# Optimization experiments

Measured on AMD Instinct MI355X. Metric: run time of the kernel, lower is better.

The kernel has to match this reference:

```python
import jax, jax.numpy as jnp
import numpy as np

B, C, H, W = 2, 256, 120, 240
HID = 512  # mlp_ratio=2 * embed_dim
EPS = 1e-5


def setup_inputs() -> dict:
    key = jax.random.key(0)
    ks = jax.random.split(key, 10)
    f = lambda k, shp, s=1.0: jax.random.normal(k, shp, jnp.float32) * s
    return {
        'x': f(ks[0], (B, C, H, W)),
        'gamma': f(ks[1], (C,), 0.1),
        'beta': f(ks[2], (C,), 0.1),
        'norm0_w': jnp.ones((C,), jnp.float32),
        'norm0_b': jnp.zeros((C,), jnp.float32),
        'norm1_w': jnp.ones((C,), jnp.float32),
        'norm1_b': jnp.zeros((C,), jnp.float32),
        'w_spec_r': f(ks[3], (C, C), 0.02),
        'w_spec_i': f(ks[4], (C, C), 0.02),
        'inner_w': f(ks[5], (C, C), 0.02),
        'inner_b': jnp.zeros((C,), jnp.float32),
        'mlp_w1': f(ks[6], (HID, C), 0.02),
        'mlp_b1': jnp.zeros((HID,), jnp.float32),
        'mlp_w2': f(ks[7], (C, HID), 0.02),
        'mlp_b2': jnp.zeros((C,), jnp.float32),
    }


def _inorm(x, w, b):
    # InstanceNorm2d (affine): normalize over spatial dims per (batch, channel)
    m = x.mean(axis=(2, 3), keepdims=True)
    v = x.var(axis=(2, 3), keepdims=True)
    xh = (x - m) * jax.lax.rsqrt(v + EPS)
    return xh * w[None, :, None, None] + b[None, :, None, None]


def _conv1x1(x, w, b=None):
    y = jnp.einsum('bihw,oi->bohw', x, w)
    return y if b is None else y + b[None, :, None, None]


def reference(x, gamma, beta, norm0_w, norm0_b, norm1_w, norm1_b,
              w_spec_r, w_spec_i, inner_w, inner_b,
              mlp_w1, mlp_b1, mlp_w2, mlp_b2):
    residual = x
    h = _inorm(x, norm0_w, norm0_b)
    # SpectralConv2d: rfft2 -> channel-mixing complex matmul (all modes kept,
    # hard_thresholding_fraction=1.0) -> irfft2. sparsity_threshold=0 -> no shrink.
    xf = jnp.fft.rfft2(h, norm='ortho')                     # [B,C,H,W//2+1] complex
    wc = (w_spec_r + 1j * w_spec_i).astype(xf.dtype)
    yf = jnp.einsum('bihw,io->bohw', xf, wc)
    h = jnp.fft.irfft2(yf, s=(H, W), norm='ortho')
    # inner skip (1x1 conv of residual) + GELU (linear filter branch)
    h = h + _conv1x1(residual, inner_w, inner_b)
    h = jax.nn.gelu(h, approximate=False)
    h = _inorm(h, norm1_w, norm1_b)
    # FiLM with scale=1
    h = (1.0 + gamma[None, :, None, None]) * h + beta[None, :, None, None]
    # distributed MLP: 1x1 conv -> GELU -> 1x1 conv
    h = _conv1x1(h, mlp_w1, mlp_b1)
    h = jax.nn.gelu(h, approximate=False)
    h = _conv1x1(h, mlp_w2, mlp_b2)
    # outer skip = identity
    return h + residual
```

## Files before the change

### kernel.cpp

```cpp
#include <hip/hip_runtime.h>
#include <hip/hip_bf16.h>

typedef __hip_bfloat16 bf16;
typedef short short8 __attribute__((ext_vector_type(8)));
typedef float f32x4 __attribute__((ext_vector_type(4)));

#define NB 2
#define NC 256
#define NH 120
#define NW 240
#define NHW (NH*NW)
#define NSP 16384
#define NHID 512
#define NPT 450
#define REPS 1e-5f
#define SC_W 0.06454972243679028f
#define SC_H 0.09128709291752769f
#define PI2 6.283185307179586f

__device__ __forceinline__ float gelu_f(float x){ return 0.5f*x*(1.f+erff(x*0.7071067811865476f)); }
__device__ __forceinline__ float us2f(ushort u){ union{float f; uint v;} c; c.v=((uint)u)<<16; return c.f; }
__device__ __forceinline__ ushort f2us(float f){ bf16 b=__float2bfloat16(f); return *(ushort*)&b; }

#define OFF_A0   0
#define OFF_D0   512
#define OFF_A1c  1024
#define OFF_D1c  1536
#define OFF_TWF  2048
#define OFF_THF  34816
#define OFF_THI  67584
#define OFF_TWI  100352
#define OFF_WRT  133120
#define OFF_WIT  165888
#define OFF_IWB  198656
#define OFF_W2B  231424
#define OFF_W1P  296960
#define OFF_B1P  428032
#define OFF_PS   429056
#define OFF_RA   889856
#define OFF_RB   9278464
#define WS_FLOATS 17667072ULL

#define RA0 OFF_RA
#define RA1 (OFF_RA+4194304)
#define RB0 OFF_RB
#define RB1 (OFF_RB+4194304)
#define OFF_FRE RB0
#define OFF_FIM (RB0+3932160)

__global__ __launch_bounds__(256) void k_setup(float* ws, const float* wsr, const float* wsi,
                                               const float* iw, const float* w2){
  int t = blockIdx.x*256 + threadIdx.x;
  if (t < 65536){
    int n=t>>8, w=t&255; float v=0.f;
    if(w<NW){
      if(n<121){ v = cosf(PI2*(float)((n*w)%NW)/(float)NW)*SC_W; }
      else if(n>=128 && n<249){ int k=n-128; v = -sinf(PI2*(float)((k*w)%NW)/(float)NW)*SC_W; }
    }
    ((ushort*)(ws+OFF_TWF))[t]=f2us(v); return;
  } t-=65536;
  if (t < 65536){
    int n=t>>8, j=t&255; float v=0.f;
    int h = j&127; bool im = (j>=128);
    if(h<NH){
      if(n<128){ int m=n; if(m<NH){ float sn,cs; sincosf(PI2*(float)((m*h)%NH)/(float)NH,&sn,&cs);
        v = (im? sn : cs)*SC_H; } }
      else { int m=n-128; if(m<NH){ float sn,cs; sincosf(PI2*(float)((m*h)%NH)/(float)NH,&sn,&cs);
        v = (im? cs : -sn)*SC_H; } }
    }
    ((ushort*)(ws+OFF_THF))[t]=f2us(v); return;
  } t-=65536;
  if (t < 65536){
    int n=t>>8, j=t&255; float v=0.f;
    int m = j&127; bool im = (j>=128);
    if(m<NH){
      if(n<128){ int h=n; if(h<NH){ float sn,cs; sincosf(PI2*(float)((h*m)%NH)/(float)NH,&sn,&cs);
        v = (im? -sn : cs)*SC_H; } }
      else { int h=n-128; if(h<NH){ float sn,cs; sincosf(PI2*(float)((h*m)%NH)/(float)NH,&sn,&cs);
        v = (im? cs : sn)*SC_H; } }
    }
    ((ushort*)(ws+OFF_THI))[t]=f2us(v); return;
  } t-=65536;
  if (t < 65536){
    int w=t>>8, j=t&255; float v=0.f;
    if(w<NW){
      int k = j&127; bool im = (j>=128);
      if(k<121){
        float ck = (k==0||k==120)? 1.f : 2.f;
        float sn,cs; sincosf(PI2*(float)((w*k)%NW)/(float)NW,&sn,&cs);
        v = ck*(im? -sn : cs)*SC_W;
      }
    }
    ((ushort*)(ws+OFF_TWI))[t]=f2us(v); return;
  } t-=65536;
  if (t < 65536){ int o=t>>8,i=t&255; ((ushort*)(ws+OFF_WRT))[t]=f2us(wsr[i*NC+o]); return; } t-=65536;
  if (t < 65536){ int o=t>>8,i=t&255; ((ushort*)(ws+OFF_WIT))[t]=f2us(wsi[i*NC+o]); return; } t-=65536;
  if (t < 65536){ ((ushort*)(ws+OFF_IWB))[t]=f2us(iw[t]); return; } t-=65536;
  if (t < 131072){ ((ushort*)(ws+OFF_W2B))[t]=f2us(w2[t]); return; }
}

__global__ __launch_bounds__(256) void k_stats0(const float* x, const float* n0w, const float* n0b, float* ws){
  int g = blockIdx.x, c = g & (NC-1);
  const float4* xp = (const float4*)(x + (size_t)g*NHW);
  float s=0.f, q=0.f;
  for(int i=threadIdx.x;i<NHW/4;i+=256){
    float4 v=xp[i];
    s+=v.x+v.y+v.z+v.w;
    q=fmaf(v.x,v.x,fmaf(v.y,v.y,fmaf(v.z,v.z,fmaf(v.w,v.w,q))));
  }
  __shared__ float ls[4], lq[4];
  #pragma unroll
  for(int o=32;o>0;o>>=1){ s+=__shfl_down(s,o,64); q+=__shfl_down(q,o,64); }
  int lane=threadIdx.x&63, wid=threadIdx.x>>6;
  if(!lane){ ls[wid]=s; lq[wid]=q; }
  __syncthreads();
  if(!threadIdx.x){
    s=ls[0]+ls[1]+ls[2]+ls[3]; q=lq[0]+lq[1]+lq[2]+lq[3];
    float m=s*(1.f/NHW), var=q*(1.f/NHW)-m*m;
    float r=rsqrtf(var+REPS);
    float a=r*n0w[c];
    ws[OFF_A0+g]=a; ws[OFF_D0+g]=fmaf(-m,a,n0b[c]);
  }
}

__global__ __launch_bounds__(256) void k_norm(const float* x, float* ws){
  int h = blockIdx.x, g = blockIdx.y, t = threadIdx.x;
  float a = ws[OFF_A0+g], d = ws[OFF_D0+g];
  ushort v = 0;
  if(t < NW) v = f2us(fmaf(a, x[(size_t)g*NHW + (size_t)h*NW + t], d));
  ((ushort*)(ws+RA0))[(size_t)g*30720 + (size_t)h*256 + t] = v;
}

template<int SPLIT, int EPI>
__global__ __launch_bounds__(256) void k_sgemm(const ushort* Ap0, const ushort* Ap1, const ushort* Bm,
                                               ushort* O0, ushort* O1, ushort* Ub){
  int nb = blockIdx.x*64, mb = blockIdx.y*256;
  int tid = threadIdx.x, w = tid>>6, l = tid&63, lq = l>>4, lr = l&15;
  const ushort* ar0[4]; const ushort* ar1[4]; const ushort* br[4];
  #pragma unroll
  for(int mt=0;mt<4;mt++){
    size_t r = mb + w*64 + mt*16 + lr;
    ar0[mt] = Ap0 + r*(SPLIT?128:256) + lq*8;
    ar1[mt] = SPLIT ? (Ap1 + r*128 + lq*8) : ar0[mt];
  }
  #pragma unroll
  for(int nt=0;nt<4;nt++) br[nt] = Bm + (size_t)(nb + nt*16 + lr)*256 + lq*8;
  f32x4 acc[4][4] = {};
  #pragma unroll
  for(int kk=0;kk<8;kk++){
    int k = kk*32;
    short8 af[4], bfr[4];
    #pragma unroll
    for(int mt=0;mt<4;mt++){
      const ushort* p = SPLIT ? ((k<128 ? ar0[mt] : ar1[mt]) + (k&127)) : (ar0[mt] + k);
      af[mt] = *(const short8*)p;
    }
    #pragma unroll
    for(int nt=0;nt<4;nt++) bfr[nt] = *(const short8*)(br[nt]+k);
    #pragma unroll
    for(int mt=0;mt<4;mt++)
      #pragma unroll
      for(int nt=0;nt<4;nt++)
        acc[mt][nt] = __builtin_amdgcn_mfma_f32_16x16x32_bf16(af[mt], bfr[nt], acc[mt][nt], 0,0,0);
  }
  #pragma unroll
  for(int mt=0;mt<4;mt++){
    #pragma unroll
    for(int r=0;r<4;r++){
      int m = mb + w*64 + mt*16 + lq*4 + r;
      #pragma unroll
      for(int nt=0;nt<4;nt++){
        int n = nb + nt*16 + lr;
        float v = acc[mt][nt][r];
        if (EPI==0){
          if(n<128) O0[(size_t)m*128+n] = f2us(v);
          else      O1[(size_t)m*128+n-128] = f2us(v);
        } else {
          int g = m>>7, h = m&127;
          if(h<NH && n<NW) Ub[(size_t)g*NHW + (size_t)h*NW + n] = f2us(v);
        }
      }
    }
  }
}

__global__ __launch_bounds__(256) void k_t64(const ushort* src, ushort* dst, int srows, int sgstr){
  __shared__ ushort lt[64][72];
  int g=blockIdx.z, i0=blockIdx.y*64, p0=blockIdx.x*64;
  int t=threadIdx.x, r=t>>2, q=t&3;
  int row = i0 + r;
  uint4 u0=make_uint4(0,0,0,0), u1=u0;
  if(row < srows){
    const ushort* sp = src + (size_t)g*sgstr + (size_t)row*128 + p0 + q*16;
    u0=*(const uint4*)sp; u1=*(const uint4*)(sp+8);
  }
  *(uint4*)&lt[r][q*16]=u0; *(uint4*)&lt[r][q*16+8]=u1;
  __syncthreads();
  int pr=t>>2, q2=t&3;
  union { ushort s[8]; uint4 u; } o0, o1;
  #pragma unroll
  for(int e=0;e<8;e++){ o0.s[e]=lt[q2*16+e][pr]; o1.s[e]=lt[q2*16+8+e][pr]; }
  ushort* dp = dst + (size_t)g*NSP + (size_t)(p0+pr)*128 + i0 + q2*16;
  *(uint4*)dp = o0.u; *(uint4*)(dp+8) = o1.u;
}

__global__ __launch_bounds__(256) void k_tP(const ushort* src, ushort* dst){
  __shared__ ushort lt[64][72];
  int b=blockIdx.z, i0=blockIdx.y*64, p0=blockIdx.x*64;
  int t=threadIdx.x, r=t>>2, q=t&3;
  const ushort* sp = src + (size_t)(b*NC+i0+r)*NSP + p0 + q*16;
  uint4 u0=*(const uint4*)sp, u1=*(const uint4*)(sp+8);
  *(uint4*)&lt[r][q*16]=u0; *(uint4*)&lt[r][q*16+8]=u1;
  __syncthreads();
  int pr=t>>2, q2=t&3;
  union { ushort s[8]; uint4 u; } o0, o1;
  #pragma unroll
  for(int e=0;e<8;e++){ o0.s[e]=lt[q2*16+e][pr]; o1.s[e]=lt[q2*16+8+e][pr]; }
  ushort* dp = dst + ((size_t)b*NSP + p0 + pr)*NC + i0 + q2*16;
  *(uint4*)dp = o0.u; *(uint4*)(dp+8) = o1.u;
}

__global__ __launch_bounds__(256) void k_mixg(float* ws){
  int b = blockIdx.z, p0 = blockIdx.x*32;
  int tid = threadIdx.x, w = tid>>6, l = tid&63, lq = l>>4, lr = l&15;
  const ushort* Wr = (const ushort*)(ws+OFF_WRT);
  const ushort* Wi = (const ushort*)(ws+OFF_WIT);
  const ushort* Gr = (const ushort*)(ws+RA0) + (size_t)b*NSP*NC;
  const ushort* Gi = (const ushort*)(ws+RA1) + (size_t)b*NSP*NC;
  const ushort *wrr[4], *wir[4], *brr[2], *bir[2];
  #pragma unroll
  for(int mt=0;mt<4;mt++){ size_t ro=(size_t)(w*64+mt*16+lr)*NC+lq*8; wrr[mt]=Wr+ro; wir[mt]=Wi+ro; }
  #pragma unroll
  for(int nt=0;nt<2;nt++){ size_t ro=(size_t)(p0+nt*16+lr)*NC+lq*8; brr[nt]=Gr+ro; bir[nt]=Gi+ro; }
  f32x4 aR[4][2]={}, aI[4][2]={};
  for(int k=0;k<256;k+=32){
    short8 fr[4], fi[4], fin[4], gr[2], gi[2];
    #pragma unroll
    for(int mt=0;mt<4;mt++){
      fr[mt]=*(const short8*)(wrr[mt]+k);
      fi[mt]=*(const short8*)(wir[mt]+k);
      union { short8 s; uint u[4]; } nv; nv.s=fi[mt];
      nv.u[0]^=0x80008000u; nv.u[1]^=0x80008000u; nv.u[2]^=0x80008000u; nv.u[3]^=0x80008000u;
      fin[mt]=nv.s;
    }
    #pragma unroll
    for(int nt=0;nt<2;nt++){ gr[nt]=*(const short8*)(brr[nt]+k); gi[nt]=*(const short8*)(bir[nt]+k); }
    #pragma unroll
    for(int mt=0;mt<4;mt++)
      #pragma unroll
      for(int nt=0;nt<2;nt++){
        aR[mt][nt]=__builtin_amdgcn_mfma_f32_16x16x32_bf16(fr[mt], gr[nt], aR[mt][nt],0,0,0);
        aR[mt][nt]=__builtin_amdgcn_mfma_f32_16x16x32_bf16(fin[mt],gi[nt], aR[mt][nt],0,0,0);
        aI[mt][nt]=__builtin_amdgcn_mfma_f32_16x16x32_bf16(fi[mt], gr[nt], aI[mt][nt],0,0,0);
        aI[mt][nt]=__builtin_amdgcn_mfma_f32_16x16x32_bf16(fr[mt], gi[nt], aI[mt][nt],0,0,0);
      }
  }
  ushort* Yre = (ushort*)(ws+RB0);
  ushort* Yim = (ushort*)(ws+RB1);
  #pragma unroll
  for(int mt=0;mt<4;mt++){
    #pragma unroll
    for(int r=0;r<4;r++){
      int m = w*64 + mt*16 + lq*4 + r;
      #pragma unroll
      for(int nt=0;nt<2;nt++){
        int n = p0 + nt*16 + lr;
        size_t ad = (size_t)(b*NC+m)*NSP + n;
        Yre[ad] = f2us(aR[mt][nt][r]);
        Yim[ad] = f2us(aI[mt][nt][r]);
      }
    }
  }
}

__global__ __launch_bounds__(256,2) void k_inner(float* ws, const float* x, const float* ib){
  __shared__ ushort xt[64][264];
  int b = blockIdx.z, blk = blockIdx.x, p0 = blk*64;
  int t = threadIdx.x, w = t>>6, l = t&63, lq = l>>4, lr = l&15;
  #pragma unroll 4
  for(int cc=0; cc<16; cc++){
    int c = cc*16 + (t>>4);
    int p4 = (t&15)*4;
    float4 v = *(const float4*)(x + ((size_t)(b*NC+c))*NHW + p0 + p4);
    xt[p4  ][c]=f2us(v.x); xt[p4+1][c]=f2us(v.y);
    xt[p4+2][c]=f2us(v.z); xt[p4+3][c]=f2us(v.w);
  }
  __syncthreads();
  const ushort* W = (const ushort*)(ws+OFF_IWB);
  const ushort* ar[4];
  #pragma unroll
  for(int mt=0;mt<4;mt++) ar[mt] = W + (size_t)(w*64+mt*16+lr)*256 + lq*8;
  f32x4 acc[4][4] = {};
  #pragma unroll
  for(int kk=0;kk<8;kk++){
    int k = kk*32;
    short8 af[4], bfr[4];
    #pragma unroll
    for(int mt=0;mt<4;mt++) af[mt] = *(const short8*)(ar[mt]+k);
    #pragma unroll
    for(int nt=0;nt<4;nt++) bfr[nt] = *(const short8*)&xt[nt*16+lr][k+lq*8];
    #pragma unroll
    for(int mt=0;mt<4;mt++)
      #pragma unroll
      for(int nt=0;nt<4;nt++)
        acc[mt][nt] = __builtin_amdgcn_mfma_f32_16x16x32_bf16(af[mt], bfr[nt], acc[mt][nt], 0,0,0);
  }
  __syncthreads();
  const ushort* Usp = (const ushort*)(ws+OFF_RA);
  float* PS = ws + OFF_PS + ((size_t)(b*NPT+blk))*512;
  #pragma unroll
  for(int mt=0;mt<4;mt++){
    #pragma unroll
    for(int r=0;r<4;r++){
      int m = w*64 + mt*16 + lq*4 + r;
      float bb = ib[m];
      float ss = 0.f, sq = 0.f;
      #pragma unroll
      for(int nt=0;nt<4;nt++){
        int n = p0 + nt*16 + lr;
        float uv = us2f(Usp[((size_t)(b*NC+m))*NHW + n]);
        float g = gelu_f(acc[mt][nt][r] + bb + uv);
        xt[nt*16+lr][m] = f2us(g);
        ss += g; sq = fmaf(g,g,sq);
      }
      #pragma unroll
      for(int ofs=1; ofs<16; ofs<<=1){ ss += __shfl_xor(ss, ofs, 64); sq += __shfl_xor(sq, ofs, 64); }
      if(lr==0){ PS[m] = ss; PS[256+m] = sq; }
    }
  }
  __syncthreads();
  ushort* Up = (ushort*)(ws+OFF_RB);
  #pragma unroll
  for(int pp=0; pp<4; pp++){
    int p = pp*16 + (t>>4);
    int c0 = (t&15)*16;
    uint4 w0 = *(uint4*)&xt[p][c0];
    uint4 w1v = *(uint4*)&xt[p][c0+8];
    ushort* dp = Up + ((size_t)(b*NHW + p0 + p))*256 + c0;
    *(uint4*)dp = w0; *(uint4*)(dp+8) = w1v;
  }
}

__global__ __launch_bounds__(256) void k_stats1p(const float* gamma, const float* beta,
                                                 const float* n1w, const float* n1b, float* ws){
  int g = blockIdx.x, b = g>>8, c = g&255;
  float s=0.f, q=0.f;
  for(int i=threadIdx.x;i<NPT;i+=256){
    const float* P = ws + OFF_PS + ((size_t)(b*NPT+i))*512;
    s += P[c]; q += P[256+c];
  }
  __shared__ float ls[4], lq2[4];
  #pragma unroll
  for(int o=32;o>0;o>>=1){ s+=__shfl_down(s,o,64); q+=__shfl_down(q,o,64); }
  int lane=threadIdx.x&63, wid=threadIdx.x>>6;
  if(!lane){ ls[wid]=s; lq2[wid]=q; }
  __syncthreads();
  if(!threadIdx.x){
    s=ls[0]+ls[1]+ls[2]+ls[3]; q=lq2[0]+lq2[1]+lq2[2]+lq2[3];
    float m=s*(1.f/NHW), var=q*(1.f/NHW)-m*m;
    float r=rsqrtf(var+REPS);
    float gp1 = 1.f + gamma[c];
    float wv = n1w[c];
    ws[OFF_A1c+g] = gp1*wv*r;
    ws[OFF_D1c+g] = gp1*(n1b[c] - m*r*wv) + beta[c];
  }
}

__global__ __launch_bounds__(64) void k_fold(float* ws, const float* w1, const float* b1){
  int o = blockIdx.x, b = blockIdx.y, t = threadIdx.x;
  float acc = 0.f;
  ushort* W1p = (ushort*)(ws+OFF_W1P);
  #pragma unroll
  for(int ii=0; ii<4; ii++){
    int i = ii*64 + t;
    float wv = w1[o*256+i];
    W1p[((size_t)(b*NHID+o))*256 + i] = f2us(wv * ws[OFF_A1c + b*NC + i]);
    acc = fmaf(wv, ws[OFF_D1c + b*NC + i], acc);
  }
  #pragma unroll
  for(int ofs=32; ofs; ofs>>=1) acc += __shfl_down(acc, ofs, 64);
  if(!t) ws[OFF_B1P + b*NHID + o] = acc + b1[o];
}

__global__ __launch_bounds__(256,2) void k_mlp(float* ws, const float* x, const float* b2, float* out){
  __shared__ ushort midT[64][520];
  int b = blockIdx.z, p0 = blockIdx.x*64;
  int t = threadIdx.x, w = t>>6, l = t&63, lq = l>>4, lr = l&15;
  const ushort* W1p = (const ushort*)(ws+OFF_W1P) + (size_t)b*NHID*256;
  const ushort* Up  = (const ushort*)(ws+OFF_RB);
  const ushort* ar[8]; const ushort* br[4];
  #pragma unroll
  for(int mt=0;mt<8;mt++) ar[mt] = W1p + (size_t)(w*128+mt*16+lr)*256 + lq*8;
  #pragma unroll
  for(int nt=0;nt<4;nt++) br[nt] = Up + ((size_t)(b*NHW + p0 + nt*16+lr))*256 + lq*8;
  f32x4 acc1[8][4] = {};
  #pragma unroll
  for(int kk=0;kk<8;kk++){
    int k = kk*32;
    short8 bfr[4];
    #pragma unroll
    for(int nt=0;nt<4;nt++) bfr[nt] = *(const short8*)(br[nt]+k);
    #pragma unroll
    for(int mt=0;mt<8;mt++){
      short8 af = *(const short8*)(ar[mt]+k);
      #pragma unroll
      for(int nt=0;nt<4;nt++)
        acc1[mt][nt] = __builtin_amdgcn_mfma_f32_16x16x32_bf16(af, bfr[nt], acc1[mt][nt], 0,0,0);
    }
  }
  const float* b1p = ws + OFF_B1P + b*NHID;
  #pragma unroll
  for(int mt=0;mt<8;mt++){
    #pragma unroll
    for(int r=0;r<4;r++){
      int m1 = w*128 + mt*16 + lq*4 + r;
      float bb = b1p[m1];
      #pragma unroll
      for(int nt=0;nt<4;nt++){
        int p = nt*16 + lr;
        midT[p][m1] = f2us(gelu_f(acc1[mt][nt][r] + bb));
      }
    }
  }
  __syncthreads();
  const ushort* W2 = (const ushort*)(ws+OFF_W2B);
  const ushort* a2[4];
  #pragma unroll
  for(int mt=0;mt<4;mt++) a2[mt] = W2 + (size_t)(w*64+mt*16+lr)*512 + lq*8;
  f32x4 acc2[4][4] = {};
  #pragma unroll
  for(int kk=0;kk<16;kk++){
    int k = kk*32;
    short8 af[4], bfr[4];
    #pragma unroll
    for(int mt=0;mt<4;mt++) af[mt] = *(const short8*)(a2[mt]+k);
    #pragma unroll
    for(int nt=0;nt<4;nt++) bfr[nt] = *(const short8*)&midT[nt*16+lr][k+lq*8];
    #pragma unroll
    for(int mt=0;mt<4;mt++)
      #pragma unroll
      for(int nt=0;nt<4;nt++)
        acc2[mt][nt] = __builtin_amdgcn_mfma_f32_16x16x32_bf16(af[mt], bfr[nt], acc2[mt][nt], 0,0,0);
  }
  #pragma unroll
  for(int mt=0;mt<4;mt++){
    #pragma unroll
    for(int r=0;r<4;r++){
      int om = w*64 + mt*16 + lq*4 + r;
      float bb = b2[om];
      #pragma unroll
      for(int nt=0;nt<4;nt++){
        int n = p0 + nt*16 + lr;
        size_t ad = ((size_t)(b*NC+om))*NHW + n;
        out[ad] = acc2[mt][nt][r] + bb + x[ad];
      }
    }
  }
}

extern "C" void kernel_launch(void* const* d_in, const int* in_sizes, int n_in,
                              void* d_out, int out_size, void* d_ws, size_t ws_size,
                              hipStream_t stream) {
  const float* x     = (const float*)d_in[0];
  const float* gamma = (const float*)d_in[1];
  const float* beta  = (const float*)d_in[2];
  const float* n0w   = (const float*)d_in[3];
  const float* n0b   = (const float*)d_in[4];
  const float* n1w   = (const float*)d_in[5];
  const float* n1b   = (const float*)d_in[6];
  const float* wsr   = (const float*)d_in[7];
  const float* wsi   = (const float*)d_in[8];
  const float* iw    = (const float*)d_in[9];
  const float* ib    = (const float*)d_in[10];
  const float* w1    = (const float*)d_in[11];
  const float* b1    = (const float*)d_in[12];
  const float* w2    = (const float*)d_in[13];
  const float* b2    = (const float*)d_in[14];
  float* ws = (float*)d_ws;
  float* out = (float*)d_out;
  if (ws_size < WS_FLOATS*4ULL) return;

  k_setup <<<dim3(2304), dim3(256), 0, stream>>>(ws, wsr, wsi, iw, w2);
  k_stats0<<<dim3(512),  dim3(256), 0, stream>>>(x, n0w, n0b, ws);
  k_norm  <<<dim3(120,512), dim3(256), 0, stream>>>(x, ws);
  k_sgemm<0,0><<<dim3(4,240), dim3(256), 0, stream>>>((const ushort*)(ws+RA0), (const ushort*)(ws+RA0),
      (const ushort*)(ws+OFF_TWF), (ushort*)(ws+OFF_FRE), (ushort*)(ws+OFF_FIM), nullptr);
  k_t64 <<<dim3(2,2,512), dim3(256), 0, stream>>>((const ushort*)(ws+OFF_FRE), (ushort*)(ws+RA0), NH, NH*128);
  k_t64 <<<dim3(2,2,512), dim3(256), 0, stream>>>((const ushort*)(ws+OFF_FIM), (ushort*)(ws+RA1), NH, NH*128);
  k_sgemm<1,0><<<dim3(4,256), dim3(256), 0, stream>>>((const ushort*)(ws+RA0), (const ushort*)(ws+RA1),
      (const ushort*)(ws+OFF_THF), (ushort*)(ws+RB0), (ushort*)(ws+RB1), nullptr);
  k_tP <<<dim3(256,4,2), dim3(256), 0, stream>>>((const ushort*)(ws+RB0), (ushort*)(ws+RA0));
  k_tP <<<dim3(256,4,2), dim3(256), 0, stream>>>((const ushort*)(ws+RB1), (ushort*)(ws+RA1));
  k_mixg <<<dim3(512,1,2), dim3(256), 0, stream>>>(ws);
  k_sgemm<1,0><<<dim3(4,256), dim3(256), 0, stream>>>((const ushort*)(ws+RB0), (const ushort*)(ws+RB1),
      (const ushort*)(ws+OFF_THI), (ushort*)(ws+RA0), (ushort*)(ws+RA1), nullptr);
  k_t64 <<<dim3(2,2,512), dim3(256), 0, stream>>>((const ushort*)(ws+RA0), (ushort*)(ws+RB0), 128, NSP);
  k_t64 <<<dim3(2,2,512), dim3(256), 0, stream>>>((const ushort*)(ws+RA1), (ushort*)(ws+RB1), 128, NSP);
  k_sgemm<1,1><<<dim3(4,256), dim3(256), 0, stream>>>((const ushort*)(ws+RB0), (const ushort*)(ws+RB1),
      (const ushort*)(ws+OFF_TWI), nullptr, nullptr, (ushort*)(ws+RA0));
  k_inner <<<dim3(NPT,1,2), dim3(256), 0, stream>>>(ws, x, ib);
  k_stats1p<<<dim3(512), dim3(256), 0, stream>>>(gamma, beta, n1w, n1b, ws);
  k_fold  <<<dim3(512,2), dim3(64), 0, stream>>>(ws, w1, b1);
  k_mlp   <<<dim3(NPT,1,2), dim3(256), 0, stream>>>(ws, x, b2, out);
}
```

Before: 648.8 us.

## Fuse MLP stages in registers, dropping the shared-memory intermediate

```diff
diff --git a/kernel.cpp b/kernel.cpp
--- a/kernel.cpp
+++ b/kernel.cpp
@@ -96,7 +96,12 @@
   if (t < 65536){ int o=t>>8,i=t&255; ((ushort*)(ws+OFF_WRT))[t]=f2us(wsr[i*NC+o]); return; } t-=65536;
   if (t < 65536){ int o=t>>8,i=t&255; ((ushort*)(ws+OFF_WIT))[t]=f2us(wsi[i*NC+o]); return; } t-=65536;
   if (t < 65536){ ((ushort*)(ws+OFF_IWB))[t]=f2us(iw[t]); return; } t-=65536;
-  if (t < 131072){ ((ushort*)(ws+OFF_W2B))[t]=f2us(w2[t]); return; }
+  if (t < 131072){
+    int o = t>>9, k = t&511;
+    int kp = (k & ~31) | ((k&4)<<2) | ((k>>1)&12) | (k&3);
+    ((ushort*)(ws+OFF_W2B))[t]=f2us(w2[(o<<9)+kp]);
+    return;
+  }
 }
 
 __global__ __launch_bounds__(256) void k_stats0(const float* x, const float* n0w, const float* n0b, float* ws){
@@ -382,78 +387,49 @@
   if(!t) ws[OFF_B1P + b*NHID + o] = acc + b1[o];
 }
 
-__global__ __launch_bounds__(256,2) void k_mlp(float* ws, const float* x, const float* b2, float* out){
-  __shared__ ushort midT[64][520];
+__global__ __launch_bounds__(256,4) void k_mlp(float* ws, const float* x, const float* b2, float* out){
   int b = blockIdx.z, p0 = blockIdx.x*64;
   int t = threadIdx.x, w = t>>6, l = t&63, lq = l>>4, lr = l&15;
+  int pw = p0 + w*16 + lr;
   const ushort* W1p = (const ushort*)(ws+OFF_W1P) + (size_t)b*NHID*256;
   const ushort* Up  = (const ushort*)(ws+OFF_RB);
-  const ushort* ar[8]; const ushort* br[4];
-  #pragma unroll
-  for(int mt=0;mt<8;mt++) ar[mt] = W1p + (size_t)(w*128+mt*16+lr)*256 + lq*8;
-  #pragma unroll
-  for(int nt=0;nt<4;nt++) br[nt] = Up + ((size_t)(b*NHW + p0 + nt*16+lr))*256 + lq*8;
-  f32x4 acc1[8][4] = {};
-  #pragma unroll
-  for(int kk=0;kk<8;kk++){
-    int k = kk*32;
-    short8 bfr[4];
-    #pragma unroll
-    for(int nt=0;nt<4;nt++) bfr[nt] = *(const short8*)(br[nt]+k);
-    #pragma unroll
-    for(int mt=0;mt<8;mt++){
-      short8 af = *(const short8*)(ar[mt]+k);
-      #pragma unroll
-      for(int nt=0;nt<4;nt++)
-        acc1[mt][nt] = __builtin_amdgcn_mfma_f32_16x16x32_bf16(af, bfr[nt], acc1[mt][nt], 0,0,0);
-    }
-  }
-  const float* b1p = ws + OFF_B1P + b*NHID;
-  #pragma unroll
-  for(int mt=0;mt<8;mt++){
+  const float*  b1p = ws + OFF_B1P + b*NHID;
+  const ushort* up  = Up + ((size_t)(b*NHW) + pw)*256 + lq*8;
+  const ushort* w2r = (const ushort*)(ws+OFF_W2B) + (size_t)lr*512 + lq*8;
+  f32x4 acc2[16] = {};
+  for(int c=0;c<16;c++){
+    const ushort* w1r = W1p + (size_t)(c*32 + lr)*256 + lq*8;
+    f32x4 a1[2] = {};
+    #pragma unroll
+    for(int kk=0;kk<8;kk++){
+      short8 bu  = *(const short8*)(up  + kk*32);
+      short8 a0  = *(const short8*)(w1r + kk*32);
+      short8 a1f = *(const short8*)(w1r + 16*256 + kk*32);
+      a1[0] = __builtin_amdgcn_mfma_f32_16x16x32_bf16(a0,  bu, a1[0], 0,0,0);
+      a1[1] = __builtin_amdgcn_mfma_f32_16x16x32_bf16(a1f, bu, a1[1], 0,0,0);
+    }
+    float4 bb0 = *(const float4*)(b1p + c*32      + lq*4);
+    float4 bb1 = *(const float4*)(b1p + c*32 + 16 + lq*4);
+    union { short8 s8; uint u[4]; } bf;
+    bf.u[0] = (uint)f2us(gelu_f(a1[0][0]+bb0.x)) | ((uint)f2us(gelu_f(a1[0][1]+bb0.y))<<16);
+    bf.u[1] = (uint)f2us(gelu_f(a1[0][2]+bb0.z)) | ((uint)f2us(gelu_f(a1[0][3]+bb0.w))<<16);
+    bf.u[2] = (uint)f2us(gelu_f(a1[1][0]+bb1.x)) | ((uint)f2us(gelu_f(a1[1][1]+bb1.y))<<16);
+    bf.u[3] = (uint)f2us(gelu_f(a1[1][2]+bb1.z)) | ((uint)f2us(gelu_f(a1[1][3]+bb1.w))<<16);
+    #pragma unroll
+    for(int mt=0;mt<16;mt++){
+      short8 a2 = *(const short8*)(w2r + (size_t)mt*16*512 + c*32);
+      acc2[mt] = __builtin_amdgcn_mfma_f32_16x16x32_bf16(a2, bf.s8, acc2[mt], 0,0,0);
+    }
+  }
+  #pragma unroll
+  for(int mt=0;mt<16;mt++){
+    float4 bb = *(const float4*)(b2 + mt*16 + lq*4);
+    float bbv[4] = {bb.x, bb.y, bb.z, bb.w};
     #pragma unroll
     for(int r=0;r<4;r++){
-      int m1 = w*128 + mt*16 + lq*4 + r;
-      float bb = b1p[m1];
-      #pragma unroll
-      for(int nt=0;nt<4;nt++){
-        int p = nt*16 + lr;
-        midT[p][m1] = f2us(gelu_f(acc1[mt][nt][r] + bb));
-      }
-    }
-  }
-  __syncthreads();
-  const ushort* W2 = (const ushort*)(ws+OFF_W2B);
-  const ushort* a2[4];
-  #pragma unroll
-  for(int mt=0;mt<4;mt++) a2[mt] = W2 + (size_t)(w*64+mt*16+lr)*512 + lq*8;
-  f32x4 acc2[4][4] = {};
-  #pragma unroll
-  for(int kk=0;kk<16;kk++){
-    int k = kk*32;
-    short8 af[4], bfr[4];
-    #pragma unroll
-    for(int mt=0;mt<4;mt++) af[mt] = *(const short8*)(a2[mt]+k);
-    #pragma unroll
-    for(int nt=0;nt<4;nt++) bfr[nt] = *(const short8*)&midT[nt*16+lr][k+lq*8];
-    #pragma unroll
-    for(int mt=0;mt<4;mt++)
-      #pragma unroll
-      for(int nt=0;nt<4;nt++)
-        acc2[mt][nt] = __builtin_amdgcn_mfma_f32_16x16x32_bf16(af[mt], bfr[nt], acc2[mt][nt], 0,0,0);
-  }
-  #pragma unroll
-  for(int mt=0;mt<4;mt++){
-    #pragma unroll
-    for(int r=0;r<4;r++){
-      int om = w*64 + mt*16 + lq*4 + r;
-      float bb = b2[om];
-      #pragma unroll
-      for(int nt=0;nt<4;nt++){
-        int n = p0 + nt*16 + lr;
-        size_t ad = ((size_t)(b*NC+om))*NHW + n;
-        out[ad] = acc2[mt][nt][r] + bb + x[ad];
-      }
+      int om = mt*16 + lq*4 + r;
+      size_t ad = ((size_t)(b*NC+om))*NHW + pw;
+      out[ad] = acc2[mt][r] + bbv[r] + x[ad];
     }
   }
 }
```

After: 780.3 us. +20.3%, slower.

## Halve MLP pixel tile, swizzle shared mid buffer, raise occupancy

Applied to the files above, without the earlier changes.

```diff
diff --git a/kernel.cpp b/kernel.cpp
--- a/kernel.cpp
+++ b/kernel.cpp
@@ -382,77 +382,82 @@
   if(!t) ws[OFF_B1P + b*NHID + o] = acc + b1[o];
 }
 
-__global__ __launch_bounds__(256,2) void k_mlp(float* ws, const float* x, const float* b2, float* out){
-  __shared__ ushort midT[64][520];
-  int b = blockIdx.z, p0 = blockIdx.x*64;
+__global__ __launch_bounds__(256,4) void k_mlp(float* ws, const float* x, const float* b2, float* out){
+  __shared__ ushort midT[32*512];
+  int b = blockIdx.z, p0 = blockIdx.x*32;
   int t = threadIdx.x, w = t>>6, l = t&63, lq = l>>4, lr = l&15;
+  int h7 = lr & 7;
   const ushort* W1p = (const ushort*)(ws+OFF_W1P) + (size_t)b*NHID*256;
   const ushort* Up  = (const ushort*)(ws+OFF_RB);
-  const ushort* ar[8]; const ushort* br[4];
+  const float*  b1p = ws + OFF_B1P + b*NHID;
+  const ushort* ar[8]; const ushort* br[2];
   #pragma unroll
   for(int mt=0;mt<8;mt++) ar[mt] = W1p + (size_t)(w*128+mt*16+lr)*256 + lq*8;
   #pragma unroll
-  for(int nt=0;nt<4;nt++) br[nt] = Up + ((size_t)(b*NHW + p0 + nt*16+lr))*256 + lq*8;
-  f32x4 acc1[8][4] = {};
+  for(int nt=0;nt<2;nt++) br[nt] = Up + ((size_t)(b*NHW + p0 + nt*16+lr))*256 + lq*8;
+  f32x4 acc1[8][2] = {};
   #pragma unroll
   for(int kk=0;kk<8;kk++){
     int k = kk*32;
-    short8 bfr[4];
-    #pragma unroll
-    for(int nt=0;nt<4;nt++) bfr[nt] = *(const short8*)(br[nt]+k);
+    short8 bfr[2];
+    #pragma unroll
+    for(int nt=0;nt<2;nt++) bfr[nt] = *(const short8*)(br[nt]+k);
     #pragma unroll
     for(int mt=0;mt<8;mt++){
       short8 af = *(const short8*)(ar[mt]+k);
       #pragma unroll
-      for(int nt=0;nt<4;nt++)
+      for(int nt=0;nt<2;nt++)
         acc1[mt][nt] = __builtin_amdgcn_mfma_f32_16x16x32_bf16(af, bfr[nt], acc1[mt][nt], 0,0,0);
     }
   }
-  const float* b1p = ws + OFF_B1P + b*NHID;
   #pragma unroll
   for(int mt=0;mt<8;mt++){
-    #pragma unroll
-    for(int r=0;r<4;r++){
-      int m1 = w*128 + mt*16 + lq*4 + r;
-      float bb = b1p[m1];
-      #pragma unroll
-      for(int nt=0;nt<4;nt++){
-        int p = nt*16 + lr;
-        midT[p][m1] = f2us(gelu_f(acc1[mt][nt][r] + bb));
-      }
-    }
-  }
-  __syncthreads();
-  const ushort* W2 = (const ushort*)(ws+OFF_W2B);
+    int jb = w*16 + mt*2 + (lq>>1);
+    float4 bb = *(const float4*)(b1p + w*128 + mt*16 + lq*4);
+    #pragma unroll
+    for(int nt=0;nt<2;nt++){
+      int px = nt*16 + lr;
+      uint u0 = (uint)f2us(gelu_f(acc1[mt][nt][0]+bb.x)) | ((uint)f2us(gelu_f(acc1[mt][nt][1]+bb.y))<<16);
+      uint u1 = (uint)f2us(gelu_f(acc1[mt][nt][2]+bb.z)) | ((uint)f2us(gelu_f(acc1[mt][nt][3]+bb.w))<<16);
+      uint byo = (uint)px*1024u + (uint)((jb ^ h7)<<4) + (uint)((lq&1)<<3);
+      *(uint2*)((char*)midT + byo) = make_uint2(u0, u1);
+    }
+  }
+  __syncthreads();
   const ushort* a2[4];
   #pragma unroll
-  for(int mt=0;mt<4;mt++) a2[mt] = W2 + (size_t)(w*64+mt*16+lr)*512 + lq*8;
-  f32x4 acc2[4][4] = {};
+  for(int mt=0;mt<4;mt++) a2[mt] = (const ushort*)(ws+OFF_W2B) + (size_t)(w*64+mt*16+lr)*512 + lq*8;
+  f32x4 acc2[4][2] = {};
   #pragma unroll
   for(int kk=0;kk<16;kk++){
-    int k = kk*32;
-    short8 af[4], bfr[4];
-    #pragma unroll
-    for(int mt=0;mt<4;mt++) af[mt] = *(const short8*)(a2[mt]+k);
-    #pragma unroll
-    for(int nt=0;nt<4;nt++) bfr[nt] = *(const short8*)&midT[nt*16+lr][k+lq*8];
-    #pragma unroll
-    for(int mt=0;mt<4;mt++)
-      #pragma unroll
-      for(int nt=0;nt<4;nt++)
-        acc2[mt][nt] = __builtin_amdgcn_mfma_f32_16x16x32_bf16(af[mt], bfr[nt], acc2[mt][nt], 0,0,0);
+    short8 bfr[2];
+    #pragma unroll
+    for(int nt=0;nt<2;nt++){
+      int px = nt*16 + lr;
+      int j2 = kk*4 + lq;
+      uint byo = (uint)px*1024u + (uint)((j2 ^ h7)<<4);
+      bfr[nt] = *(const short8*)((const char*)midT + byo);
+    }
+    #pragma unroll
+    for(int mt=0;mt<4;mt++){
+      short8 af = *(const short8*)(a2[mt]+kk*32);
+      #pragma unroll
+      for(int nt=0;nt<2;nt++)
+        acc2[mt][nt] = __builtin_amdgcn_mfma_f32_16x16x32_bf16(af, bfr[nt], acc2[mt][nt], 0,0,0);
+    }
   }
   #pragma unroll
   for(int mt=0;mt<4;mt++){
+    float4 bb = *(const float4*)(b2 + w*64 + mt*16 + lq*4);
+    float bbv[4] = {bb.x, bb.y, bb.z, bb.w};
     #pragma unroll
     for(int r=0;r<4;r++){
       int om = w*64 + mt*16 + lq*4 + r;
-      float bb = b2[om];
-      #pragma unroll
-      for(int nt=0;nt<4;nt++){
+      #pragma unroll
+      for(int nt=0;nt<2;nt++){
         int n = p0 + nt*16 + lr;
         size_t ad = ((size_t)(b*NC+om))*NHW + n;
-        out[ad] = acc2[mt][nt][r] + bb + x[ad];
+        out[ad] = acc2[mt][nt][r] + bbv[r] + x[ad];
       }
     }
   }
@@ -501,5 +506,5 @@
   k_inner <<<dim3(NPT,1,2), dim3(256), 0, stream>>>(ws, x, ib);
   k_stats1p<<<dim3(512), dim3(256), 0, stream>>>(gamma, beta, n1w, n1b, ws);
   k_fold  <<<dim3(512,2), dim3(64), 0, stream>>>(ws, w1, b1);
-  k_mlp   <<<dim3(NPT,1,2), dim3(256), 0, stream>>>(ws, x, b2, out);
-}
+  k_mlp   <<<dim3(900,1,2), dim3(256), 0, stream>>>(ws, x, b2, out);
+}
```

Result: slower. 678.6 us (+4.6%).

## Split fused MLP into two LDS-tiled 128x128 GEMMs with async global-to-LDS loads

Applied to the files above, without the earlier changes.

```diff
diff --git a/kernel.cpp b/kernel.cpp
--- a/kernel.cpp
+++ b/kernel.cpp
@@ -21,6 +21,12 @@
 __device__ __forceinline__ float gelu_f(float x){ return 0.5f*x*(1.f+erff(x*0.7071067811865476f)); }
 __device__ __forceinline__ float us2f(ushort u){ union{float f; uint v;} c; c.v=((uint)u)<<16; return c.f; }
 __device__ __forceinline__ ushort f2us(float f){ bf16 b=__float2bfloat16(f); return *(ushort*)&b; }
+
+typedef __attribute__((address_space(3))) void lds_void;
+typedef const __attribute__((address_space(1))) void gbl_void;
+__device__ __forceinline__ void gload16(const ushort* g, ushort* l){
+  __builtin_amdgcn_global_load_lds((gbl_void*)g, (lds_void*)l, 16, 0, 0);
+}
 
 #define OFF_A0   0
 #define OFF_D0   512
@@ -382,79 +388,73 @@
   if(!t) ws[OFF_B1P + b*NHID + o] = acc + b1[o];
 }
 
-__global__ __launch_bounds__(256,2) void k_mlp(float* ws, const float* x, const float* b2, float* out){
-  __shared__ ushort midT[64][520];
-  int b = blockIdx.z, p0 = blockIdx.x*64;
+template<int KD, int EPI>
+__global__ __launch_bounds__(256) void k_gemm128(const ushort* __restrict__ A, const ushort* __restrict__ B,
+                                                 const float* __restrict__ bias, const float* __restrict__ xres,
+                                                 ushort* __restrict__ Obf, float* __restrict__ Ofl){
+  __shared__ ushort As[2][4096] __attribute__((aligned(16)));
+  __shared__ ushort Bs[2][4096] __attribute__((aligned(16)));
   int t = threadIdx.x, w = t>>6, l = t&63, lq = l>>4, lr = l&15;
-  const ushort* W1p = (const ushort*)(ws+OFF_W1P) + (size_t)b*NHID*256;
-  const ushort* Up  = (const ushort*)(ws+OFF_RB);
-  const ushort* ar[8]; const ushort* br[4];
-  #pragma unroll
-  for(int mt=0;mt<8;mt++) ar[mt] = W1p + (size_t)(w*128+mt*16+lr)*256 + lq*8;
-  #pragma unroll
-  for(int nt=0;nt<4;nt++) br[nt] = Up + ((size_t)(b*NHW + p0 + nt*16+lr))*256 + lq*8;
-  f32x4 acc1[8][4] = {};
-  #pragma unroll
-  for(int kk=0;kk<8;kk++){
-    int k = kk*32;
-    short8 bfr[4];
-    #pragma unroll
-    for(int nt=0;nt<4;nt++) bfr[nt] = *(const short8*)(br[nt]+k);
-    #pragma unroll
-    for(int mt=0;mt<8;mt++){
-      short8 af = *(const short8*)(ar[mt]+k);
+  int wr = w>>1, wc = w&1;
+  int nb = blockIdx.x*128, mb = blockIdx.y*128;
+  const ushort* Ab = A + (size_t)mb*KD;
+  const ushort* Bb = B + (size_t)nb*KD;
+  int srow = t>>2;
+  int scg  = (t&3) ^ ((t>>3)&3);
+  size_t so0 = (size_t)srow*KD + scg*8;
+  size_t so1 = (size_t)(srow+64)*KD + scg*8;
+  int ld0 = w*512, ld1 = 2048 + w*512;
+  int swk = (lq ^ ((lr>>1)&3))*8;
+  f32x4 acc[4][4] = {};
+  gload16(Ab+so0, &As[0][ld0]); gload16(Ab+so1, &As[0][ld1]);
+  gload16(Bb+so0, &Bs[0][ld0]); gload16(Bb+so1, &Bs[0][ld1]);
+  const int NK = KD/32;
+  for(int kt=0; kt<NK; kt++){
+    int cur = kt&1;
+    __syncthreads();
+    if(kt+1 < NK){
+      size_t ko = (size_t)(kt+1)*32;
+      gload16(Ab+so0+ko, &As[cur^1][ld0]); gload16(Ab+so1+ko, &As[cur^1][ld1]);
+      gload16(Bb+so0+ko, &Bs[cur^1][ld0]); gload16(Bb+so1+ko, &Bs[cur^1][ld1]);
+    }
+    short8 af[4], bfr[4];
+    #pragma unroll
+    for(int mt=0;mt<4;mt++) af[mt]  = *(const short8*)&As[cur][(wr*64+mt*16+lr)*32 + swk];
+    #pragma unroll
+    for(int nt=0;nt<4;nt++) bfr[nt] = *(const short8*)&Bs[cur][(wc*64+nt*16+lr)*32 + swk];
+    #pragma unroll
+    for(int mt=0;mt<4;mt++)
       #pragma unroll
       for(int nt=0;nt<4;nt++)
-        acc1[mt][nt] = __builtin_amdgcn_mfma_f32_16x16x32_bf16(af, bfr[nt], acc1[mt][nt], 0,0,0);
-    }
-  }
-  const float* b1p = ws + OFF_B1P + b*NHID;
-  #pragma unroll
-  for(int mt=0;mt<8;mt++){
-    #pragma unroll
-    for(int r=0;r<4;r++){
-      int m1 = w*128 + mt*16 + lq*4 + r;
-      float bb = b1p[m1];
-      #pragma unroll
-      for(int nt=0;nt<4;nt++){
-        int p = nt*16 + lr;
-        midT[p][m1] = f2us(gelu_f(acc1[mt][nt][r] + bb));
+        acc[mt][nt] = __builtin_amdgcn_mfma_f32_16x16x32_bf16(af[mt], bfr[nt], acc[mt][nt], 0,0,0);
+  }
+  if (EPI==0){
+    #pragma unroll
+    for(int nt=0;nt<4;nt++){
+      int n = nb + wc*64 + nt*16 + lr;
+      float bb = bias[n];
+      #pragma unroll
+      for(int mt=0;mt<4;mt++)
+        #pragma unroll
+        for(int r=0;r<4;r++){
+          int m = mb + wr*64 + mt*16 + lq*4 + r;
+          Obf[(size_t)m*NHID + n] = f2us(gelu_f(acc[mt][nt][r] + bb));
+        }
+    }
+  } else {
+    #pragma unroll
+    for(int mt=0;mt<4;mt++)
+      #pragma unroll
+      for(int r=0;r<4;r++){
+        int m = mb + wr*64 + mt*16 + lq*4 + r;
+        float bb = bias[m];
+        #pragma unroll
+        for(int nt=0;nt<4;nt++){
+          int n = nb + wc*64 + nt*16 + lr;
+          size_t ad = (size_t)m*NHW + n;
+          Ofl[ad] = acc[mt][nt][r] + bb + xres[ad];
+        }
       }
-    }
-  }
-  __syncthreads();
-  const ushort* W2 = (const ushort*)(ws+OFF_W2B);
-  const ushort* a2[4];
-  #pragma unroll
-  for(int mt=0;mt<4;mt++) a2[mt] = W2 + (size_t)(w*64+mt*16+lr)*512 + lq*8;
-  f32x4 acc2[4][4] = {};
-  #pragma unroll
-  for(int kk=0;kk<16;kk++){
-    int k = kk*32;
-    short8 af[4], bfr[4];
-    #pragma unroll
-    for(int mt=0;mt<4;mt++) af[mt] = *(const short8*)(a2[mt]+k);
-    #pragma unroll
-    for(int nt=0;nt<4;nt++) bfr[nt] = *(const short8*)&midT[nt*16+lr][k+lq*8];
-    #pragma unroll
-    for(int mt=0;mt<4;mt++)
-      #pragma unroll
-      for(int nt=0;nt<4;nt++)
-        acc2[mt][nt] = __builtin_amdgcn_mfma_f32_16x16x32_bf16(af[mt], bfr[nt], acc2[mt][nt], 0,0,0);
-  }
-  #pragma unroll
-  for(int mt=0;mt<4;mt++){
-    #pragma unroll
-    for(int r=0;r<4;r++){
-      int om = w*64 + mt*16 + lq*4 + r;
-      float bb = b2[om];
-      #pragma unroll
-      for(int nt=0;nt<4;nt++){
-        int n = p0 + nt*16 + lr;
-        size_t ad = ((size_t)(b*NC+om))*NHW + n;
-        out[ad] = acc2[mt][nt][r] + bb + x[ad];
-      }
-    }
   }
 }
 
@@ -501,5 +501,15 @@
   k_inner <<<dim3(NPT,1,2), dim3(256), 0, stream>>>(ws, x, ib);
   k_stats1p<<<dim3(512), dim3(256), 0, stream>>>(gamma, beta, n1w, n1b, ws);
   k_fold  <<<dim3(512,2), dim3(64), 0, stream>>>(ws, w1, b1);
-  k_mlp   <<<dim3(NPT,1,2), dim3(256), 0, stream>>>(ws, x, b2, out);
-}
+  ushort* mid = (ushort*)(ws+OFF_RA);
+  for(int b=0;b<2;b++){
+    k_gemm128<256,0><<<dim3(4,225), dim3(256), 0, stream>>>(
+        (const ushort*)(ws+OFF_RB) + (size_t)b*NHW*256,
+        (const ushort*)(ws+OFF_W1P) + (size_t)b*NHID*256,
+        ws+OFF_B1P + b*NHID, nullptr, mid, nullptr);
+    k_gemm128<512,1><<<dim3(225,2), dim3(256), 0, stream>>>(
+        (const ushort*)(ws+OFF_W2B),
+        mid,
+        b2, x + (size_t)b*NC*NHW, nullptr, out + (size_t)b*NC*NHW);
+  }
+}
```

Result: no change. 643.9 us (-0.8%).
